# Optimization experiments

Measured on AMD Instinct MI355X. Metric: run time of the kernel, lower is better.

Reference implementation:

```python
import jax, jax.numpy as jnp
import numpy as np
from jax.scipy.special import betaln

V, E, H, Z = 50000, 300, 200, 30  # vocab, emb, enc hidden, z_rnn_size
B, T = 64, 512
L, R = -0.1, 1.1  # HardKuma stretched support


def setup_inputs() -> dict:
    key = jax.random.key(0)
    ks = jax.random.split(key, 16)
    s = 0.05  # weight scale to keep gates in a sane range
    return {
        "x": jax.random.randint(ks[0], (B, T), 0, V),
        "mask": jnp.ones((B, T), dtype=bool),
        "emb_W": jax.random.normal(ks[1], (V, E), jnp.float32) * 0.1,
        "enc_Wi_f": jax.random.normal(ks[2], (E, 4 * H), jnp.float32) * s,
        "enc_Wh_f": jax.random.normal(ks[3], (H, 4 * H), jnp.float32) * s,
        "enc_b_f": jnp.zeros((4 * H,), jnp.float32),
        "enc_Wi_b": jax.random.normal(ks[4], (E, 4 * H), jnp.float32) * s,
        "enc_Wh_b": jax.random.normal(ks[5], (H, 4 * H), jnp.float32) * s,
        "enc_b_b": jnp.zeros((4 * H,), jnp.float32),
        "z_Wi": jax.random.normal(ks[6], (2 * H + 1, 4 * Z), jnp.float32) * s,
        "z_Wh": jax.random.normal(ks[7], (Z, 4 * Z), jnp.float32) * s,
        "z_b": jnp.zeros((4 * Z,), jnp.float32),
        "kuma_Wa": jax.random.normal(ks[8], (2 * H + Z, 1), jnp.float32) * s,
        "kuma_ba": jnp.zeros((1,), jnp.float32),
        "kuma_Wb": jax.random.normal(ks[9], (2 * H + Z, 1), jnp.float32) * s,
        "kuma_bb": jnp.zeros((1,), jnp.float32),
    }


def _lstm_scan(xt, Wi, Wh, b, reverse):
    # xt: [T, B, E] -> outputs h: [T, B, H]; torch gate order i, f, g, o
    Bsz = xt.shape[1]
    Hd = Wh.shape[0]
    x_proj = xt @ Wi + b  # precompute input projection [T, B, 4H]

    def step(carry, xp):
        h, c = carry
        g = xp + h @ Wh
        i, f, gg, o = jnp.split(g, 4, axis=-1)
        c = jax.nn.sigmoid(f) * c + jax.nn.sigmoid(i) * jnp.tanh(gg)
        h = jax.nn.sigmoid(o) * jnp.tanh(c)
        return (h, c), h

    init = (jnp.zeros((Bsz, Hd), xt.dtype), jnp.zeros((Bsz, Hd), xt.dtype))
    _, hs = jax.lax.scan(step, init, x_proj, reverse=reverse)
    return hs


def reference(x, mask, emb_W, enc_Wi_f, enc_Wh_f, enc_b_f, enc_Wi_b, enc_Wh_b,
              enc_b_b, z_Wi, z_Wh, z_b, kuma_Wa, kuma_ba, kuma_Wb, kuma_bb):
    # eval-mode forward (dropout = identity, deterministic HardKuma branch)
    emb = emb_W[x]                       # [B, T, E]
    xt = emb.transpose(1, 0, 2)          # [T, B, E]
    hf = _lstm_scan(xt, enc_Wi_f, enc_Wh_f, enc_b_f, False)
    hb = _lstm_scan(xt, enc_Wi_b, enc_Wh_b, enc_b_b, True)
    h = jnp.concatenate([hf, hb], axis=-1)  # [T, B, 2H]

    x0 = (0.0 - L) / (R - L)
    x1 = (1.0 - L) / (R - L)

    def step(carry, h_t):
        zh, zc = carry                    # LSTMCell state, each [B, Z]
        gin = jnp.concatenate([h_t, zh], axis=-1)  # [B, 2H+Z]
        a = jnp.clip(jax.nn.softplus(gin @ kuma_Wa + kuma_ba), 1e-6, 100.0)
        b = jnp.clip(jax.nn.softplus(gin @ kuma_Wb + kuma_bb), 1e-6, 100.0)
        # HardKuma point masses: p0 = F(x0), p1 = 1 - F(x1); F(x)=1-(1-x^a)^b
        p0 = 1.0 - (1.0 - x0 ** a) ** b
        p1 = (1.0 - x1 ** a) ** b
        pc = 1.0 - p0 - p1
        kmean = jnp.exp(betaln(1.0 + 1.0 / a, b) + jnp.log(b))  # Kuma mean
        smean = L + (R - L) * kmean       # stretched mean
        zero_one = jnp.where(p0 > p1, 0.0, 1.0)
        z_t = jnp.where((pc > p0) & (pc > p1), smean, zero_one)  # [B, 1]
        rnn_in = jnp.concatenate([h_t, z_t], axis=-1)  # [B, 2H+1]
        g = rnn_in @ z_Wi + zh @ z_Wh + z_b
        i, f, gg, o = jnp.split(g, 4, axis=-1)
        zc = jax.nn.sigmoid(f) * zc + jax.nn.sigmoid(i) * jnp.tanh(gg)
        zh = jax.nn.sigmoid(o) * jnp.tanh(zc)
        return (zh, zc), z_t[:, 0]

    Bsz = h.shape[1]
    init = (jnp.zeros((Bsz, Z), h.dtype), jnp.zeros((Bsz, Z), h.dtype))
    _, zs = jax.lax.scan(step, init, h)   # zs: [T, B]
    z = zs.T                              # [B, T]
    return jnp.where(mask, z, 0.0)
```

## Files before the change

kernel.cpp:

```cpp
#include <hip/hip_runtime.h>


#define T_LEN 512
#define NBATCH 64
#define EMB 300
#define HID 200

typedef __attribute__((ext_vector_type(2))) _Float16 half2v;
typedef __attribute__((ext_vector_type(8))) _Float16 f16x8;
typedef __attribute__((ext_vector_type(4))) float f32x4;

union HU16 { _Float16 h; unsigned short u; };
union U32H2 { unsigned int u; half2v h; };

__device__ __forceinline__ half2v h2_from_u32(unsigned int u) { U32H2 v; v.u = u; return v.h; }
__device__ __forceinline__ unsigned int u32_from_h2(half2v h) { U32H2 v; v.h = h; return v.u; }
__device__ __forceinline__ half2v h2_pack(float a, float b) {
  half2v h; h.x = (_Float16)a; h.y = (_Float16)b; return h;
}
__device__ __forceinline__ float fdot2f(half2v a, half2v b, float c) {
#if __has_builtin(__builtin_amdgcn_fdot2)
  return __builtin_amdgcn_fdot2(a, b, c, false);
#else
  return (float)a.x * (float)b.x + (float)a.y * (float)b.y + c;
#endif
}
__device__ __forceinline__ float sigmf(float x) { return 1.0f / (1.0f + __expf(-x)); }
__device__ __forceinline__ float tanhfast(float x) {
  float ax = fabsf(x);
  float t = __expf(-2.0f * ax);
  float r = (1.0f - t) / (1.0f + t);
  return x < 0.0f ? -r : r;
}
__device__ __forceinline__ float softplus_fast(float x) {
  return fmaxf(x, 0.0f) + __logf(1.0f + __expf(-fabsf(x)));
}
__device__ __forceinline__ float lgamma_pos6(float z) {
  const float w = z + 6.0f;
  const float prod = z * (z + 1.f) * (z + 2.f) * (z + 3.f) * (z + 4.f) * (z + 5.f);
  const float iw = 1.0f / w;
  const float iw2 = iw * iw;
  const float ser = iw * (0.0833333333f + iw2 * (-0.00277777778f + iw2 * 0.000793650794f));
  return (w - 0.5f) * __logf(w) - w + 0.91893853320467f + ser - __logf(prod);
}
__device__ __forceinline__ float hardkuma_z(float apre, float bpre) {
  const float a = fminf(fmaxf(softplus_fast(apre), 1e-6f), 100.0f);
  const float b = fminf(fmaxf(softplus_fast(bpre), 1e-6f), 100.0f);
  const float lx0 = -2.48490664979f;
  const float lx1 = -0.08701137698f;
  const float u0 = __expf(a * lx0) - 1.0f;
  const float p0 = 1.0f - __expf(b * __logf(-u0));
  const float u1 = __expf(a * lx1) - 1.0f;
  const float p1 = __expf(b * __logf(-u1));
  const float pc = 1.0f - p0 - p1;
  const float ia = 1.0f / a;
  const float lbeta = lgamma_pos6(1.0f + ia) + lgamma_pos6(b) - lgamma_pos6(1.0f + ia + b);
  const float kmean = __expf(lbeta + __logf(b));
  const float smean = -0.1f + 1.2f * kmean;
  const float zo = (p0 > p1) ? 0.0f : 1.0f;
  return (pc > p0 && pc > p1) ? smean : zo;
}

__global__ __launch_bounds__(256) void wit_kernel(
    const float* __restrict__ WiF, const float* __restrict__ WiB, _Float16* __restrict__ WiT)
{
  const int o = blockIdx.x * 256 + threadIdx.x;
  const int dir = o / (896 * 320);
  const int rem = o - dir * 896 * 320;
  const int n = rem / 320;
  const int k = rem - n * 320;
  const float* Wi = dir ? WiB : WiF;
  float v = (n < 800 && k < EMB) ? Wi[(size_t)k * 800 + n] : 0.0f;
  WiT[o] = (_Float16)v;
}

__global__ __launch_bounds__(320) void abuf_kernel(
    const int* __restrict__ xids, const float* __restrict__ embW, _Float16* __restrict__ Abuf)
{
  const int r = blockIdx.x;
  const int t = r >> 6;
  const int b = r & 63;
  const int k = threadIdx.x;
  const size_t row = (size_t)xids[b * T_LEN + t];
  float v = (k < EMB) ? embW[row * EMB + k] : 0.0f;
  Abuf[(size_t)r * 320 + k] = (_Float16)v;
}

__global__ __launch_bounds__(256) void proj_kernel(
    const _Float16* __restrict__ Abuf, const _Float16* __restrict__ WiT,
    const float* __restrict__ biasF, const float* __restrict__ biasB,
    _Float16* __restrict__ xp)
{
  const int t = blockIdx.x;
  const int nbase = blockIdx.y * 128;
  const int dir = blockIdx.z;
  const float* bias = dir ? biasB : biasF;

  const int tid = threadIdx.x;
  const int w = tid >> 6;
  const int lane = tid & 63;
  const int m16 = lane & 15;
  const int q = lane >> 4;

  f32x4 acc[8];
#pragma unroll
  for (int i = 0; i < 8; ++i) acc[i] = (f32x4){0.f, 0.f, 0.f, 0.f};

  const _Float16* arow = Abuf + ((size_t)t * 64 + w * 16 + m16) * 320;
  const _Float16* bbase = WiT + ((size_t)dir * 896) * 320;

  for (int kt = 0; kt < 10; ++kt) {
    const int kk = kt * 32 + q * 8;
    const f16x8 af = *(const f16x8*)(arow + kk);
#pragma unroll
    for (int nt = 0; nt < 8; ++nt) {
      const f16x8 bf = *(const f16x8*)(bbase + (size_t)(nbase + nt * 16 + m16) * 320 + kk);
      acc[nt] = __builtin_amdgcn_mfma_f32_16x16x32_f16(af, bf, acc[nt], 0, 0, 0);
    }
  }
#pragma unroll
  for (int nt = 0; nt < 8; ++nt) {
    const int cg = nbase + nt * 16 + m16;
    if (cg < 800) {
      const float bv = bias[cg];
#pragma unroll
      for (int reg = 0; reg < 4; ++reg) {
        const int brow = w * 16 + q * 4 + reg;
        xp[((size_t)(dir * 64 + brow) * T_LEN + t) * 800 + cg] = (_Float16)(acc[nt][reg] + bv);
      }
    }
  }
}

__global__ __launch_bounds__(512, 1) void lstm_kernel(
    const float* __restrict__ WhF, const float* __restrict__ WhB,
    const _Float16* __restrict__ xp, _Float16* __restrict__ hout)
{
  const int chain = blockIdx.x;
  const int b = chain & 63;
  const int dir = chain >> 6;
  const float* Wh = dir ? WhB : WhF;
  const int tid = threadIdx.x;
  const int m = tid & 255;
  const int half = tid >> 8;
  const bool active = m < HID;

  __shared__ __align__(16) unsigned short h16[208];
  __shared__ __align__(16) float part[HID * 4];

  half2v w[4][52];
  if (active) {
#pragma unroll
    for (int g = 0; g < 4; ++g) {
      const float* wc = Wh + g * HID + m;
#pragma unroll
      for (int p = 0; p < 52; ++p) {
        const int k = 2 * (half * 52 + p);
        const float w0 = (k < HID) ? wc[(size_t)k * 800] : 0.0f;
        const float w1 = (k + 1 < HID) ? wc[(size_t)(k + 1) * 800] : 0.0f;
        w[g][p] = h2_pack(w0, w1);
      }
    }
  }
  if (tid < 104) ((unsigned int*)h16)[tid] = 0;

  float cst = 0.0f;
  const _Float16* xprow = xp + (size_t)(dir * 64 + b) * T_LEN * 800;

  _Float16 xc0 = (_Float16)0.f, xc1 = (_Float16)0.f, xc2 = (_Float16)0.f, xc3 = (_Float16)0.f;
  if (active && half == 0) {
    const _Float16* xpt = xprow + (size_t)(dir ? (T_LEN - 1) : 0) * 800 + m;
    xc0 = xpt[0]; xc1 = xpt[200]; xc2 = xpt[400]; xc3 = xpt[600];
  }
  __syncthreads();

  const int base = half * 13;
  for (int s = 0; s < T_LEN; ++s) {
    const int t = dir ? (T_LEN - 1 - s) : s;
    _Float16 xn0 = xc0, xn1 = xc1, xn2 = xc2, xn3 = xc3;
    if (active && half == 0 && (s + 1) < T_LEN) {
      const int tn = dir ? (t - 1) : (t + 1);
      const _Float16* xpt = xprow + (size_t)tn * 800 + m;
      xn0 = xpt[0]; xn1 = xpt[200]; xn2 = xpt[400]; xn3 = xpt[600];
    }
    float a0 = 0.f, a1 = 0.f, a2 = 0.f, a3 = 0.f;
    if (active) {
      const uint4* h4 = (const uint4*)h16;
#define DOT4(HP, IDX) \
      a0 = fdot2f(HP, w[0][IDX], a0); \
      a1 = fdot2f(HP, w[1][IDX], a1); \
      a2 = fdot2f(HP, w[2][IDX], a2); \
      a3 = fdot2f(HP, w[3][IDX], a3);
#pragma unroll
      for (int pp = 0; pp < 13; ++pp) {
        const uint4 hc = h4[base + pp];
        const half2v hp0 = h2_from_u32(hc.x);
        const half2v hp1 = h2_from_u32(hc.y);
        const half2v hp2 = h2_from_u32(hc.z);
        const half2v hp3 = h2_from_u32(hc.w);
        DOT4(hp0, 4 * pp + 0)
        DOT4(hp1, 4 * pp + 1)
        DOT4(hp2, 4 * pp + 2)
        DOT4(hp3, 4 * pp + 3)
      }
#undef DOT4
      if (half) *(float4*)&part[4 * m] = (float4){a0, a1, a2, a3};
    }
    __syncthreads();
    if (active && half == 0) {
      const float4 pr = *(const float4*)&part[4 * m];
      a0 += pr.x + (float)xc0;
      a1 += pr.y + (float)xc1;
      a2 += pr.z + (float)xc2;
      a3 += pr.w + (float)xc3;
      const float gi = sigmf(a0), gf = sigmf(a1), gg = tanhfast(a2), go = sigmf(a3);
      cst = gf * cst + gi * gg;
      const float hm = go * tanhfast(cst);
      HU16 hu; hu.h = (_Float16)hm;
      h16[m] = hu.u;
      hout[((size_t)t * 64 + b) * 400 + dir * HID + m] = hu.h;
      xc0 = xn0; xc1 = xn1; xc2 = xn2; xc3 = xn3;
    }
    __syncthreads();
  }
}

__global__ __launch_bounds__(256) void bt_kernel(
    const float* __restrict__ kWa, const float* __restrict__ kWb,
    const float* __restrict__ zWi, _Float16* __restrict__ BT)
{
  const int o = blockIdx.x * 256 + threadIdx.x;
  const int n = o / 416;
  const int k = o - n * 416;
  float v = 0.0f;
  if (k < 400) {
    if (n == 0) v = kWa[k];
    else if (n == 1) v = kWb[k];
    else if (n < 122) v = zWi[(size_t)k * 120 + (n - 2)];
  }
  BT[o] = (_Float16)v;
}

__global__ __launch_bounds__(256, 1) void pre_gemm(
    const _Float16* __restrict__ hout, const _Float16* __restrict__ BT,
    float* __restrict__ pre)
{
  const int bid = blockIdx.x;
  const int tid = threadIdx.x;
  const int w = tid >> 6;
  const int lane = tid & 63;
  const int m16 = lane & 15;
  const int q = lane >> 4;

  __shared__ __align__(16) unsigned short bt_lds[128 * 424];
#pragma unroll
  for (int it = 0; it < 26; ++it) {
    const int f = tid + 256 * it;
    const int n = f / 52;
    const int koct = f - n * 52;
    *(uint4*)&bt_lds[n * 424 + koct * 8] = *(const uint4*)&BT[(size_t)n * 416 + koct * 8];
  }
  __syncthreads();

  f32x4 acc[8];
#pragma unroll
  for (int i = 0; i < 8; ++i) acc[i] = (f32x4){0.f, 0.f, 0.f, 0.f};

  const _Float16* arow = hout + ((size_t)bid * 64 + w * 16 + m16) * 400;
#pragma unroll
  for (int kf = 0; kf < 13; ++kf) {
    const int kk = kf * 32 + q * 8;
    const int ka = (kk < 400) ? kk : 0;
    const f16x8 af = *(const f16x8*)(arow + ka);
#pragma unroll
    for (int nt = 0; nt < 8; ++nt) {
      const f16x8 bf = *(const f16x8*)&bt_lds[(nt * 16 + m16) * 424 + kk];
      acc[nt] = __builtin_amdgcn_mfma_f32_16x16x32_f16(af, bf, acc[nt], 0, 0, 0);
    }
  }
#pragma unroll
  for (int nt = 0; nt < 8; ++nt) {
    const int col = nt * 16 + m16;
#pragma unroll
    for (int reg = 0; reg < 4; ++reg) {
      const int row = w * 16 + q * 4 + reg;
      pre[((size_t)bid * 64 + row) * 128 + col] = acc[nt][reg];
    }
  }
}

__global__ __launch_bounds__(64, 1) void zscan_kernel(
    const float* __restrict__ pre,
    const float* __restrict__ zWi, const float* __restrict__ zWh, const float* __restrict__ zb,
    const float* __restrict__ kWa, const float* __restrict__ kba,
    const float* __restrict__ kWb, const float* __restrict__ kbb,
    float* __restrict__ out)
{
  const int b = blockIdx.x;
  const int l = threadIdx.x;

  half2v wzhA[15], wzhB[15];
  float zbA = 0.f, zbB = 0.f, wzA = 0.f, wzB = 0.f;
#pragma unroll
  for (int k = 0; k < 15; ++k) { wzhA[k] = h2_pack(0.f, 0.f); wzhB[k] = h2_pack(0.f, 0.f); }
  if (l < 60) {
    const int j0 = 2 * l, j1 = 2 * l + 1;
#pragma unroll
    for (int k = 0; k < 15; ++k) {
      wzhA[k] = h2_pack(zWh[(size_t)(2 * k) * 120 + j0], zWh[(size_t)(2 * k + 1) * 120 + j0]);
      wzhB[k] = h2_pack(zWh[(size_t)(2 * k) * 120 + j1], zWh[(size_t)(2 * k + 1) * 120 + j1]);
    }
    zbA = zb[j0]; zbB = zb[j1];
    wzA = zWi[(size_t)400 * 120 + j0]; wzB = zWi[(size_t)400 * 120 + j1];
  }
  half2v kw2 = h2_pack(0.f, 0.f);
  const int kidx = l & 15;
  if (l < 31 && kidx < 15) {
    const float* kw = (l < 16) ? kWa : kWb;
    kw2 = h2_pack(kw[400 + 2 * kidx], kw[400 + 2 * kidx + 1]);
  }
  const float kbaS = kba[0], kbbS = kbb[0];

  float zc = 0.f, zh = 0.f;
  unsigned int zhp = u32_from_h2(h2_pack(0.f, 0.f));

  const float* prow = pre + (size_t)b * 128;
  float2 gpre = {0.f, 0.f};
  if (l <= 60) {
    const int off = (l < 60) ? (2 + 2 * l) : 0;
    gpre = *(const float2*)(prow + off);
  }

  for (int t = 0; t < T_LEN; ++t) {
    const float2 cur = gpre;
    const float preA = __shfl(cur.x, 60);
    const float preB = __shfl(cur.y, 60);
    if ((t + 1) < T_LEN && l <= 60) {
      const int off = (l < 60) ? (2 + 2 * l) : 0;
      gpre = *(const float2*)(prow + (size_t)(t + 1) * 64 * 128 + off);
    }
    const unsigned int z2k = (unsigned int)__shfl((int)zhp, 2 * kidx);
    float pk = fdot2f(h2_from_u32(z2k), kw2, 0.0f);
    pk += __shfl_xor(pk, 1);
    pk += __shfl_xor(pk, 2);
    pk += __shfl_xor(pk, 4);
    pk += __shfl_xor(pk, 8);
    const float apre = __shfl(pk, 0) + preA + kbaS;
    const float bpre = __shfl(pk, 16) + preB + kbbS;
    const float zt = hardkuma_z(apre, bpre);
    if (l == 0) out[(size_t)b * T_LEN + t] = zt;

    float gA = cur.x + zbA + wzA * zt;
    float gB = cur.y + zbB + wzB * zt;
#pragma unroll
    for (int k = 0; k < 15; ++k) {
      const unsigned int z2 = (unsigned int)__shfl((int)zhp, 2 * k);
      const half2v h2 = h2_from_u32(z2);
      gA = fdot2f(h2, wzhA[k], gA);
      gB = fdot2f(h2, wzhB[k], gB);
    }
    const int mm = (l < 30) ? l : 0;
    float gv[4];
#pragma unroll
    for (int c4 = 0; c4 < 4; ++c4) {
      const int c = mm + 30 * c4;
      const float vx = __shfl(gA, c >> 1);
      const float vy = __shfl(gB, c >> 1);
      gv[c4] = (c & 1) ? vy : vx;
    }
    if (l < 30) {
      zc = sigmf(gv[1]) * zc + sigmf(gv[0]) * tanhfast(gv[2]);
      zh = sigmf(gv[3]) * tanhfast(zc);
    }
    const float zhn = __shfl_xor(zh, 1);
    zhp = u32_from_h2(h2_pack(zh, zhn));
  }
}

extern "C" void kernel_launch(void* const* d_in, const int* in_sizes, int n_in,
                              void* d_out, int out_size, void* d_ws, size_t ws_size,
                              hipStream_t stream)
{
  const int*   x    = (const int*)d_in[0];
  const float* embW = (const float*)d_in[2];
  const float* WiF  = (const float*)d_in[3];
  const float* WhF  = (const float*)d_in[4];
  const float* bF   = (const float*)d_in[5];
  const float* WiB  = (const float*)d_in[6];
  const float* WhB  = (const float*)d_in[7];
  const float* bB   = (const float*)d_in[8];
  const float* zWi  = (const float*)d_in[9];
  const float* zWh  = (const float*)d_in[10];
  const float* zb   = (const float*)d_in[11];
  const float* kWa  = (const float*)d_in[12];
  const float* kba  = (const float*)d_in[13];
  const float* kWb  = (const float*)d_in[14];
  const float* kbb  = (const float*)d_in[15];
  float* out = (float*)d_out;

  char* ws = (char*)d_ws;
  _Float16* xp   = (_Float16*)ws;
  _Float16* WiT  = (_Float16*)(ws + 104857600);
  _Float16* Abuf = (_Float16*)(ws + 106004480);
  _Float16* hout = (_Float16*)(ws + 104857600);
  _Float16* BT   = (_Float16*)ws;
  float*    pre  = (float*)(ws + 33554432);

  wit_kernel <<<dim3(2240), 256, 0, stream>>>(WiF, WiB, WiT);
  abuf_kernel<<<dim3(32768), 320, 0, stream>>>(x, embW, Abuf);
  proj_kernel<<<dim3(T_LEN, 7, 2), 256, 0, stream>>>(Abuf, WiT, bF, bB, xp);
  lstm_kernel<<<dim3(128), 512, 0, stream>>>(WhF, WhB, xp, hout);
  bt_kernel  <<<dim3(208), 256, 0, stream>>>(kWa, kWb, zWi, BT);
  pre_gemm   <<<dim3(T_LEN), 256, 0, stream>>>(hout, BT, pre);
  zscan_kernel<<<dim3(NBATCH), 64, 0, stream>>>(pre, zWi, zWh, zb, kWa, kba, kWb, kbb, out);
}
```

Measured before the change: 1.912 ms.

## Remap LSTM and z-scan recurrences to gate-column threads and drop LDS staging

The encoder LSTM recurrence now gives each of 400 threads two full gate columns with all 200 hidden inputs held in registers. This replaces the split-K layout that needed a partial-sum exchange, though gate pairs still pass through shared memory. The z-scan kernel gives each of 30 cell lanes its own four gates and computes the Kuma projections redundantly in every lane, cutting the cross-lane shuffles per step. The pre_gemm kernel reads B fragments directly from global memory instead of staging them in LDS. These changes raise register pressure (200 packed weights per thread) and add redundant arithmetic in exchange for fewer syncs and shuffles on the serial critical path.

```diff
diff --git a/kernel.cpp b/kernel.cpp
--- a/kernel.cpp
+++ b/kernel.cpp
@@ -14,7 +14,6 @@
 union U32H2 { unsigned int u; half2v h; };
 
 __device__ __forceinline__ half2v h2_from_u32(unsigned int u) { U32H2 v; v.u = u; return v.h; }
-__device__ __forceinline__ unsigned int u32_from_h2(half2v h) { U32H2 v; v.h = h; return v.u; }
 __device__ __forceinline__ half2v h2_pack(float a, float b) {
   half2v h; h.x = (_Float16)a; h.y = (_Float16)b; return h;
 }
@@ -132,7 +131,8 @@
   }
 }
 
-__global__ __launch_bounds__(512, 1) void lstm_kernel(
+__global__ __attribute__((amdgpu_flat_work_group_size(512, 512), amdgpu_waves_per_eu(2, 2)))
+void lstm_kernel(
     const float* __restrict__ WhF, const float* __restrict__ WhB,
     const _Float16* __restrict__ xp, _Float16* __restrict__ hout)
 {
@@ -140,87 +140,79 @@
   const int b = chain & 63;
   const int dir = chain >> 6;
   const float* Wh = dir ? WhB : WhF;
-  const int tid = threadIdx.x;
-  const int m = tid & 255;
-  const int half = tid >> 8;
-  const bool active = m < HID;
-
-  __shared__ __align__(16) unsigned short h16[208];
-  __shared__ __align__(16) float part[HID * 4];
-
-  half2v w[4][52];
+  const int g = threadIdx.x;
+  const bool active = g < 400;
+  const int c0 = g, c1 = g + 400;
+
+  __shared__ __align__(16) unsigned short h16[HID];
+  __shared__ float fo0[HID];
+  __shared__ float fo1[HID];
+
+  half2v w0[100], w1[100];
   if (active) {
 #pragma unroll
-    for (int g = 0; g < 4; ++g) {
-      const float* wc = Wh + g * HID + m;
-#pragma unroll
-      for (int p = 0; p < 52; ++p) {
-        const int k = 2 * (half * 52 + p);
-        const float w0 = (k < HID) ? wc[(size_t)k * 800] : 0.0f;
-        const float w1 = (k + 1 < HID) ? wc[(size_t)(k + 1) * 800] : 0.0f;
-        w[g][p] = h2_pack(w0, w1);
-      }
-    }
-  }
-  if (tid < 104) ((unsigned int*)h16)[tid] = 0;
+    for (int p = 0; p < 100; ++p) {
+      w0[p] = h2_pack(Wh[(size_t)(2 * p) * 800 + c0], Wh[(size_t)(2 * p + 1) * 800 + c0]);
+      w1[p] = h2_pack(Wh[(size_t)(2 * p) * 800 + c1], Wh[(size_t)(2 * p + 1) * 800 + c1]);
+    }
+  }
+  if (g < 100) ((unsigned int*)h16)[g] = 0;
 
   float cst = 0.0f;
   const _Float16* xprow = xp + (size_t)(dir * 64 + b) * T_LEN * 800;
 
-  _Float16 xc0 = (_Float16)0.f, xc1 = (_Float16)0.f, xc2 = (_Float16)0.f, xc3 = (_Float16)0.f;
-  if (active && half == 0) {
-    const _Float16* xpt = xprow + (size_t)(dir ? (T_LEN - 1) : 0) * 800 + m;
-    xc0 = xpt[0]; xc1 = xpt[200]; xc2 = xpt[400]; xc3 = xpt[600];
+  float x0 = 0.f, x1 = 0.f;
+  if (active) {
+    const _Float16* xpt = xprow + (size_t)(dir ? (T_LEN - 1) : 0) * 800;
+    x0 = (float)xpt[c0]; x1 = (float)xpt[c1];
   }
   __syncthreads();
 
-  const int base = half * 13;
   for (int s = 0; s < T_LEN; ++s) {
     const int t = dir ? (T_LEN - 1 - s) : s;
-    _Float16 xn0 = xc0, xn1 = xc1, xn2 = xc2, xn3 = xc3;
-    if (active && half == 0 && (s + 1) < T_LEN) {
+    float xn0 = x0, xn1 = x1;
+    if (active && (s + 1) < T_LEN) {
       const int tn = dir ? (t - 1) : (t + 1);
-      const _Float16* xpt = xprow + (size_t)tn * 800 + m;
-      xn0 = xpt[0]; xn1 = xpt[200]; xn2 = xpt[400]; xn3 = xpt[600];
-    }
-    float a0 = 0.f, a1 = 0.f, a2 = 0.f, a3 = 0.f;
+      const _Float16* xpt = xprow + (size_t)tn * 800;
+      xn0 = (float)xpt[c0]; xn1 = (float)xpt[c1];
+    }
+    float d0 = 0.f, d0b = 0.f, d1 = 0.f, d1b = 0.f;
     if (active) {
       const uint4* h4 = (const uint4*)h16;
-#define DOT4(HP, IDX) \
-      a0 = fdot2f(HP, w[0][IDX], a0); \
-      a1 = fdot2f(HP, w[1][IDX], a1); \
-      a2 = fdot2f(HP, w[2][IDX], a2); \
-      a3 = fdot2f(HP, w[3][IDX], a3);
-#pragma unroll
-      for (int pp = 0; pp < 13; ++pp) {
-        const uint4 hc = h4[base + pp];
-        const half2v hp0 = h2_from_u32(hc.x);
-        const half2v hp1 = h2_from_u32(hc.y);
-        const half2v hp2 = h2_from_u32(hc.z);
-        const half2v hp3 = h2_from_u32(hc.w);
-        DOT4(hp0, 4 * pp + 0)
-        DOT4(hp1, 4 * pp + 1)
-        DOT4(hp2, 4 * pp + 2)
-        DOT4(hp3, 4 * pp + 3)
+#pragma unroll
+      for (int pp = 0; pp < 25; ++pp) {
+        const uint4 hc = h4[pp];
+        const half2v ha = h2_from_u32(hc.x);
+        const half2v hb = h2_from_u32(hc.y);
+        const half2v hcx = h2_from_u32(hc.z);
+        const half2v hd = h2_from_u32(hc.w);
+        d0  = fdot2f(ha,  w0[4 * pp + 0], d0);
+        d0b = fdot2f(hb,  w0[4 * pp + 1], d0b);
+        d0  = fdot2f(hcx, w0[4 * pp + 2], d0);
+        d0b = fdot2f(hd,  w0[4 * pp + 3], d0b);
+        d1  = fdot2f(ha,  w1[4 * pp + 0], d1);
+        d1b = fdot2f(hb,  w1[4 * pp + 1], d1b);
+        d1  = fdot2f(hcx, w1[4 * pp + 2], d1);
+        d1b = fdot2f(hd,  w1[4 * pp + 3], d1b);
       }
-#undef DOT4
-      if (half) *(float4*)&part[4 * m] = (float4){a0, a1, a2, a3};
+      if (g >= 200) {
+        fo0[g - 200] = d0 + d0b + x0;
+        fo1[g - 200] = d1 + d1b + x1;
+      }
     }
     __syncthreads();
-    if (active && half == 0) {
-      const float4 pr = *(const float4*)&part[4 * m];
-      a0 += pr.x + (float)xc0;
-      a1 += pr.y + (float)xc1;
-      a2 += pr.z + (float)xc2;
-      a3 += pr.w + (float)xc3;
-      const float gi = sigmf(a0), gf = sigmf(a1), gg = tanhfast(a2), go = sigmf(a3);
+    if (g < 200) {
+      const float gi = sigmf(d0 + d0b + x0);
+      const float gg = tanhfast(d1 + d1b + x1);
+      const float gf = sigmf(fo0[g]);
+      const float go = sigmf(fo1[g]);
       cst = gf * cst + gi * gg;
       const float hm = go * tanhfast(cst);
       HU16 hu; hu.h = (_Float16)hm;
-      h16[m] = hu.u;
-      hout[((size_t)t * 64 + b) * 400 + dir * HID + m] = hu.h;
-      xc0 = xn0; xc1 = xn1; xc2 = xn2; xc3 = xn3;
-    }
+      h16[g] = hu.u;
+      hout[((size_t)t * 64 + b) * 400 + dir * HID + g] = hu.h;
+    }
+    x0 = xn0; x1 = xn1;
     __syncthreads();
   }
 }
@@ -252,16 +244,6 @@
   const int m16 = lane & 15;
   const int q = lane >> 4;
 
-  __shared__ __align__(16) unsigned short bt_lds[128 * 424];
-#pragma unroll
-  for (int it = 0; it < 26; ++it) {
-    const int f = tid + 256 * it;
-    const int n = f / 52;
-    const int koct = f - n * 52;
-    *(uint4*)&bt_lds[n * 424 + koct * 8] = *(const uint4*)&BT[(size_t)n * 416 + koct * 8];
-  }
-  __syncthreads();
-
   f32x4 acc[8];
 #pragma unroll
   for (int i = 0; i < 8; ++i) acc[i] = (f32x4){0.f, 0.f, 0.f, 0.f};
@@ -274,7 +256,7 @@
     const f16x8 af = *(const f16x8*)(arow + ka);
 #pragma unroll
     for (int nt = 0; nt < 8; ++nt) {
-      const f16x8 bf = *(const f16x8*)&bt_lds[(nt * 16 + m16) * 424 + kk];
+      const f16x8 bf = *(const f16x8*)(BT + (size_t)(nt * 16 + m16) * 416 + kk);
       acc[nt] = __builtin_amdgcn_mfma_f32_16x16x32_f16(af, bf, acc[nt], 0, 0, 0);
     }
   }
@@ -289,7 +271,8 @@
   }
 }
 
-__global__ __launch_bounds__(64, 1) void zscan_kernel(
+__global__ __attribute__((amdgpu_flat_work_group_size(64, 64), amdgpu_waves_per_eu(1, 1)))
+void zscan_kernel(
     const float* __restrict__ pre,
     const float* __restrict__ zWi, const float* __restrict__ zWh, const float* __restrict__ zb,
     const float* __restrict__ kWa, const float* __restrict__ kba,
@@ -298,82 +281,86 @@
 {
   const int b = blockIdx.x;
   const int l = threadIdx.x;
-
-  half2v wzhA[15], wzhB[15];
-  float zbA = 0.f, zbB = 0.f, wzA = 0.f, wzB = 0.f;
-#pragma unroll
-  for (int k = 0; k < 15; ++k) { wzhA[k] = h2_pack(0.f, 0.f); wzhB[k] = h2_pack(0.f, 0.f); }
-  if (l < 60) {
-    const int j0 = 2 * l, j1 = 2 * l + 1;
-#pragma unroll
-    for (int k = 0; k < 15; ++k) {
-      wzhA[k] = h2_pack(zWh[(size_t)(2 * k) * 120 + j0], zWh[(size_t)(2 * k + 1) * 120 + j0]);
-      wzhB[k] = h2_pack(zWh[(size_t)(2 * k) * 120 + j1], zWh[(size_t)(2 * k + 1) * 120 + j1]);
-    }
-    zbA = zb[j0]; zbB = zb[j1];
-    wzA = zWi[(size_t)400 * 120 + j0]; wzB = zWi[(size_t)400 * 120 + j1];
-  }
-  half2v kw2 = h2_pack(0.f, 0.f);
-  const int kidx = l & 15;
-  if (l < 31 && kidx < 15) {
-    const float* kw = (l < 16) ? kWa : kWb;
-    kw2 = h2_pack(kw[400 + 2 * kidx], kw[400 + 2 * kidx + 1]);
+  const bool cell = l < 30;
+
+  half2v wg[4][15];
+  float zb4[4] = {0.f, 0.f, 0.f, 0.f}, wz4[4] = {0.f, 0.f, 0.f, 0.f};
+#pragma unroll
+  for (int j = 0; j < 4; ++j) {
+    const int col = cell ? (l + 30 * j) : 0;
+#pragma unroll
+    for (int p = 0; p < 15; ++p) {
+      const float wa = zWh[(size_t)(2 * p) * 120 + col];
+      const float wb = zWh[(size_t)(2 * p + 1) * 120 + col];
+      wg[j][p] = cell ? h2_pack(wa, wb) : h2_pack(0.f, 0.f);
+    }
+    if (cell) { zb4[j] = zb[col]; wz4[j] = zWi[(size_t)400 * 120 + col]; }
+  }
+  half2v kwa[15], kwb[15];
+#pragma unroll
+  for (int p = 0; p < 15; ++p) {
+    kwa[p] = h2_pack(kWa[400 + 2 * p], kWa[400 + 2 * p + 1]);
+    kwb[p] = h2_pack(kWb[400 + 2 * p], kWb[400 + 2 * p + 1]);
   }
   const float kbaS = kba[0], kbbS = kbb[0];
 
-  float zc = 0.f, zh = 0.f;
-  unsigned int zhp = u32_from_h2(h2_pack(0.f, 0.f));
+  float zc = 0.f, zhf = 0.f;
 
   const float* prow = pre + (size_t)b * 128;
-  float2 gpre = {0.f, 0.f};
-  if (l <= 60) {
-    const int off = (l < 60) ? (2 + 2 * l) : 0;
-    gpre = *(const float2*)(prow + off);
+  float pv[4];
+  float pk0, pk1;
+  {
+    const int lc = cell ? l : 0;
+#pragma unroll
+    for (int j = 0; j < 4; ++j) pv[j] = prow[2 + lc + 30 * j];
+    pk0 = prow[0]; pk1 = prow[1];
   }
 
   for (int t = 0; t < T_LEN; ++t) {
-    const float2 cur = gpre;
-    const float preA = __shfl(cur.x, 60);
-    const float preB = __shfl(cur.y, 60);
-    if ((t + 1) < T_LEN && l <= 60) {
-      const int off = (l < 60) ? (2 + 2 * l) : 0;
-      gpre = *(const float2*)(prow + (size_t)(t + 1) * 64 * 128 + off);
-    }
-    const unsigned int z2k = (unsigned int)__shfl((int)zhp, 2 * kidx);
-    float pk = fdot2f(h2_from_u32(z2k), kw2, 0.0f);
-    pk += __shfl_xor(pk, 1);
-    pk += __shfl_xor(pk, 2);
-    pk += __shfl_xor(pk, 4);
-    pk += __shfl_xor(pk, 8);
-    const float apre = __shfl(pk, 0) + preA + kbaS;
-    const float bpre = __shfl(pk, 16) + preB + kbbS;
-    const float zt = hardkuma_z(apre, bpre);
+    float cur[4];
+#pragma unroll
+    for (int j = 0; j < 4; ++j) cur[j] = cell ? pv[j] : 0.f;
+    const float ck0 = pk0, ck1 = pk1;
+    if ((t + 1) < T_LEN) {
+      const float* prn = prow + (size_t)(t + 1) * 64 * 128;
+      const int lc = cell ? l : 0;
+#pragma unroll
+      for (int j = 0; j < 4; ++j) pv[j] = prn[2 + lc + 30 * j];
+      pk0 = prn[0]; pk1 = prn[1];
+    }
+    half2v zhp[15];
+#pragma unroll
+    for (int p = 0; p < 15; ++p) {
+      const float ze = __shfl(zhf, 2 * p);
+      const float zo = __shfl(zhf, 2 * p + 1);
+      zhp[p] = h2_pack(ze, zo);
+    }
+    float aa = ck0 + kbaS, ab = 0.f, ba = ck1 + kbbS, bb = 0.f;
+#pragma unroll
+    for (int p = 0; p < 15; p += 2) {
+      aa = fdot2f(zhp[p], kwa[p], aa);
+      ba = fdot2f(zhp[p], kwb[p], ba);
+      if (p + 1 < 15) {
+        ab = fdot2f(zhp[p + 1], kwa[p + 1], ab);
+        bb = fdot2f(zhp[p + 1], kwb[p + 1], bb);
+      }
+    }
+    const float zt = hardkuma_z(aa + ab, ba + bb);
     if (l == 0) out[(size_t)b * T_LEN + t] = zt;
 
-    float gA = cur.x + zbA + wzA * zt;
-    float gB = cur.y + zbB + wzB * zt;
-#pragma unroll
-    for (int k = 0; k < 15; ++k) {
-      const unsigned int z2 = (unsigned int)__shfl((int)zhp, 2 * k);
-      const half2v h2 = h2_from_u32(z2);
-      gA = fdot2f(h2, wzhA[k], gA);
-      gB = fdot2f(h2, wzhB[k], gB);
-    }
-    const int mm = (l < 30) ? l : 0;
-    float gv[4];
-#pragma unroll
-    for (int c4 = 0; c4 < 4; ++c4) {
-      const int c = mm + 30 * c4;
-      const float vx = __shfl(gA, c >> 1);
-      const float vy = __shfl(gB, c >> 1);
-      gv[c4] = (c & 1) ? vy : vx;
-    }
-    if (l < 30) {
-      zc = sigmf(gv[1]) * zc + sigmf(gv[0]) * tanhfast(gv[2]);
-      zh = sigmf(gv[3]) * tanhfast(zc);
-    }
-    const float zhn = __shfl_xor(zh, 1);
-    zhp = u32_from_h2(h2_pack(zh, zhn));
+    float gq[4];
+#pragma unroll
+    for (int j = 0; j < 4; ++j) {
+      float s0 = cur[j] + zb4[j], s1 = 0.f;
+#pragma unroll
+      for (int p = 0; p < 15; p += 2) {
+        s0 = fdot2f(zhp[p], wg[j][p], s0);
+        if (p + 1 < 15) s1 = fdot2f(zhp[p + 1], wg[j][p + 1], s1);
+      }
+      gq[j] = s0 + s1 + wz4[j] * zt;
+    }
+    zc = sigmf(gq[1]) * zc + sigmf(gq[0]) * tanhfast(gq[2]);
+    zhf = sigmf(gq[3]) * tanhfast(zc);
   }
 }
 
```

After: 1.903 ms. About the same (-0.5%).
